# Performance work log

Measured on AMD Instinct MI355X. Metric: run time of the kernel, lower is better.

Reference implementation:

```python
import jax, jax.numpy as jnp
import numpy as np
from jax import lax

NB = 3          # num_fft_bins
BETA_SCALE = 0.1


def _conv(x, w, b):
    # x: [B,Ci,H,W], w: [Co,Ci,3,3] (torch OIHW), b: [Co]
    y = lax.conv_general_dilated(x, w, (1, 1), 'SAME',
                                 dimension_numbers=('NCHW', 'OIHW', 'NCHW'))
    return y + b[None, :, None, None]


def _global_mean_std(x):
    # x: [B,C,H,W] -> mean,std over C*H*W, unbiased std (torch default ddof=1)
    B = x.shape[0]
    xf = x.reshape(B, -1)
    return jnp.mean(xf, axis=1), jnp.std(xf, axis=1, ddof=1)


def _row_fft_features(x):
    # x: [B,C,H,W] -> [B,NB]
    B, C, H, W = x.shape
    spec = jnp.fft.rfft(x.reshape(B, C * H, W), axis=-1)
    power = spec.real ** 2 + spec.imag ** 2       # [B, C*H, F]
    pm = jnp.mean(power, axis=1)                  # [B, F]
    F = pm.shape[-1]
    bs = F // NB
    feats = []
    for k in range(NB):
        s = k * bs
        e = (k + 1) * bs if k < NB - 1 else F
        feats.append(jnp.mean(pm[:, s:e], axis=-1))
    feats = jnp.log1p(jnp.stack(feats, axis=1))   # [B, NB]
    return feats / (jnp.mean(feats, axis=1, keepdims=True) + 1e-6)


def reference(noisy, base_out, mem_clean, w1, b1, w2, b2, w3, b3, mw1, mb1, mw2, mb2):
    C = noisy.shape[1]
    # local residual CNN on [noisy, base_out]
    h = jax.nn.relu(_conv(jnp.concatenate([noisy, base_out], axis=1), w1, b1))
    h = jax.nn.relu(_conv(h, w2, b2))
    r = _conv(h, w3, b3)                          # [B,C,H,W]

    # hyper features: 6 global stats + 3*NB fft band features
    mn, sn = _global_mean_std(noisy)
    mb_, sb = _global_mean_std(base_out)
    mm, sm = _global_mean_std(mem_clean)
    feats = jnp.concatenate([
        jnp.stack([mn, sn, mb_, sb, mm, sm], axis=1),
        _row_fft_features(noisy),
        _row_fft_features(base_out),
        _row_fft_features(mem_clean),
    ], axis=1)                                    # [B, 6+3*NB]

    hid = jax.nn.relu(feats @ mw1.T + mb1)
    hyper = hid @ mw2.T + mb2                     # [B, 2C]
    gamma = jax.nn.sigmoid(hyper[:, :C])[:, :, None, None]
    beta = (BETA_SCALE * jnp.tanh(hyper[:, C:]))[:, :, None, None]

    out = base_out + gamma * r + beta
    return jnp.clip(out, 0.0, 1.0)


def setup_inputs() -> dict:
    key = jax.random.key(0)
    ks = jax.random.split(key, 16)
    B, C, H, W = 32, 1, 512, 512
    Hc = 16
    in_feat = 6 + 3 * NB
    s = 0.05
    return {
        'noisy': jax.random.uniform(ks[0], (B, C, H, W), jnp.float32),
        'base_out': jax.random.uniform(ks[1], (B, C, H, W), jnp.float32),
        'mem_clean': jax.random.uniform(ks[2], (B, C, H, W), jnp.float32),
        'w1': jax.random.normal(ks[3], (Hc, 2 * C, 3, 3), jnp.float32) * s,
        'b1': jax.random.normal(ks[4], (Hc,), jnp.float32) * s,
        'w2': jax.random.normal(ks[5], (Hc, Hc, 3, 3), jnp.float32) * s,
        'b2': jax.random.normal(ks[6], (Hc,), jnp.float32) * s,
        'w3': jax.random.normal(ks[7], (C, Hc, 3, 3), jnp.float32) * s,
        'b3': jax.random.normal(ks[8], (C,), jnp.float32) * s,
        'mw1': jax.random.normal(ks[9], (Hc, in_feat), jnp.float32) * s,
        'mb1': jax.random.normal(ks[10], (Hc,), jnp.float32) * s,
        'mw2': jax.random.normal(ks[11], (2 * C, Hc), jnp.float32) * s,
        'mb2': jax.random.normal(ks[12], (2 * C,), jnp.float32) * s,
    }
```

## Files before the change

kernel.cpp:

```cpp
#include <hip/hip_runtime.h>
#include <stdint.h>

typedef _Float16 h8_t __attribute__((ext_vector_type(8)));
typedef _Float16 h4_t __attribute__((ext_vector_type(4)));
typedef float f32x4 __attribute__((ext_vector_type(4)));

union H8 { h8_t v; uint32_t u[4]; _Float16 h[8]; };
union H4 { h4_t v; uint32_t u[2]; _Float16 h[4]; };

struct TrueT  { static constexpr bool value = true;  };
struct FalseT { static constexpr bool value = false; };

#define S1 584
#define S2 552


__global__ void zero_ws(double* wsd) {
    int i = threadIdx.x;
    if (i < 480)
        __hip_atomic_store(&wsd[i], 0.0, __ATOMIC_RELAXED, __HIP_MEMORY_SCOPE_AGENT);
}

__global__ __launch_bounds__(512) void fft_stats(const float* __restrict__ noisy,
                                                 const float* __restrict__ base,
                                                 const float* __restrict__ mem,
                                                 double* __restrict__ binacc,
                                                 double* __restrict__ stats) {
    int bid = blockIdx.x;
    int tid = threadIdx.x;
    int f   = tid >> 8;
    int t   = tid & 255;
    int rp  = ((bid & 127) << 1) | f;
    int b   = (bid >> 7) & 31;
    int iid = bid >> 12;
    const float* x = (iid == 0) ? noisy : (iid == 1) ? base : mem;
    const float* rowA = x + (((size_t)b << 9) + (rp << 1)) * 512;
    const float* rowB = rowA + 512;

    __shared__ float re[1024], im[1024];
    __shared__ float2 tw[256];
    __shared__ float sbins[3];
    __shared__ float swsum[8], swsq[8];
    const int fb = f << 9;

    if (tid < 256) {
        float ang = -6.2831853071795864769f * (float)tid * (1.f / 512.f);
        float sn, cs;
        __sincosf(ang, &sn, &cs);
        tw[tid] = make_float2(cs, sn);
    }

    float a0 = rowA[t], a1 = rowA[t + 256];
    float b0 = rowB[t], b1 = rowB[t + 256];

    int r0 = __brev((unsigned)t) >> 23;
    int r1 = __brev((unsigned)(t + 256)) >> 23;
    re[fb + r0] = a0; im[fb + r0] = b0;
    re[fb + r1] = a1; im[fb + r1] = b1;

    float ps = a0 + a1 + b0 + b1;
    float pq = a0 * a0 + a1 * a1 + b0 * b0 + b1 * b1;
    #pragma unroll
    for (int off = 32; off > 0; off >>= 1) {
        ps += __shfl_down(ps, off);
        pq += __shfl_down(pq, off);
    }
    if ((tid & 63) == 0) { swsum[tid >> 6] = ps; swsq[tid >> 6] = pq; }
    if (tid < 3) sbins[tid] = 0.f;
    __syncthreads();

    for (int s = 1; s <= 9; ++s) {
        int h = 1 << (s - 1);
        int pos = t & (h - 1);
        int grp = t >> (s - 1);
        int i0 = fb + (grp << s) + pos;
        int i1 = i0 + h;
        float2 w = tw[pos << (9 - s)];
        float cs = w.x, sn = w.y;
        float xr = re[i1], xi = im[i1];
        float tr = xr * cs - xi * sn;
        float ti = xr * sn + xi * cs;
        float ur = re[i0], ui = im[i0];
        re[i1] = ur - tr; im[i1] = ui - ti;
        re[i0] = ur + tr; im[i0] = ui + ti;
        __syncthreads();
    }

    for (int fq = t; fq <= 256; fq += 256) {
        int nf = (512 - fq) & 511;
        float zr = re[fb + fq], zi = im[fb + fq];
        float yr = re[fb + nf], yi = im[fb + nf];
        float ar = 0.5f * (zr + yr), ai = 0.5f * (zi - yi);
        float br = 0.5f * (zi + yi), bi = -0.5f * (zr - yr);
        float pw = ar * ar + ai * ai + br * br + bi * bi;
        int bin = (fq < 85) ? 0 : ((fq < 170) ? 1 : 2);
        atomicAdd(&sbins[bin], pw);
    }
    __syncthreads();
    if (tid < 3) atomicAdd(&binacc[(iid * 32 + b) * 3 + tid], (double)sbins[tid]);
    if (tid == 0) {
        float s8 = 0.f, q8 = 0.f;
        #pragma unroll
        for (int i = 0; i < 8; ++i) { s8 += swsum[i]; q8 += swsq[i]; }
        atomicAdd(&stats[(iid * 32 + b) * 2 + 0], (double)s8);
        atomicAdd(&stats[(iid * 32 + b) * 2 + 1], (double)q8);
    }
}

__global__ __launch_bounds__(256, 2) void conv_fused(
    const float* __restrict__ noisy, const float* __restrict__ base,
    const float* __restrict__ w1, const float* __restrict__ b1,
    const float* __restrict__ w2, const float* __restrict__ b2,
    const float* __restrict__ w3, const float* __restrict__ b3,
    const double* __restrict__ binacc, const double* __restrict__ stats,
    const float* __restrict__ mw1, const float* __restrict__ mb1,
    const float* __restrict__ mw2, const float* __restrict__ mb2,
    float* __restrict__ out) {

    __shared__ _Float16 sH1[36 * S1 + 32];
    __shared__ _Float16 sH2[34 * S2 + 32];
    __shared__ float sMLP[18];
    _Float16* sIn = sH2;

    const int tid = threadIdx.x;
    const int bid = blockIdx.x;
    const int bx = bid & 15, by = (bid >> 4) & 15, b = bid >> 8;
    const int oy0 = by * 32, ox0 = bx * 32;
    const int l = tid & 63, wave = tid >> 6;
    const int g = l >> 4, c15 = l & 15;
    const int t1 = g >> 1, e8 = (g & 1) << 3;
    const bool interior = ((unsigned)(bx - 1) < 14u) && ((unsigned)(by - 1) < 14u);

    if (tid < 16) {
        float feats[15];
        const double N = 262144.0;
        #pragma unroll
        for (int i = 0; i < 3; ++i) {
            const double* sp = &stats[(i * 32 + b) * 2];
            double s = __hip_atomic_load(&sp[0], __ATOMIC_RELAXED, __HIP_MEMORY_SCOPE_AGENT);
            double q = __hip_atomic_load(&sp[1], __ATOMIC_RELAXED, __HIP_MEMORY_SCOPE_AGENT);
            double mean = s / N;
            double var = (q - s * s / N) / (N - 1.0);
            feats[2 * i]     = (float)mean;
            feats[2 * i + 1] = sqrtf(fmaxf((float)var, 0.f));
        }
        const double cnt[3] = {85.0, 85.0, 87.0};
        #pragma unroll
        for (int i = 0; i < 3; ++i) {
            float fv[3]; float m = 0.f;
            #pragma unroll
            for (int k = 0; k < 3; ++k) {
                const double* bp = &binacc[(i * 32 + b) * 3 + k];
                double bv = __hip_atomic_load(bp, __ATOMIC_RELAXED, __HIP_MEMORY_SCOPE_AGENT);
                fv[k] = log1pf((float)(bv / (512.0 * cnt[k])));
                m += fv[k];
            }
            m = m * (1.f / 3.f);
            #pragma unroll
            for (int k = 0; k < 3; ++k) feats[6 + i * 3 + k] = fv[k] / (m + 1e-6f);
        }
        float a = mb1[tid];
        #pragma unroll
        for (int j = 0; j < 15; ++j) a += mw1[tid * 15 + j] * feats[j];
        sMLP[tid] = fmaxf(a, 0.f);
    }

    H8 wf1; H8 wf2[5]; H8 wf3[5];
    #pragma unroll
    for (int i = 0; i < 8; ++i) {
        int k = 8 * g + i;
        float wv = 0.f;
        if (k < 18) wv = w1[c15 * 18 + (k & 1) * 9 + (k >> 1)];
        wf1.h[i] = (_Float16)wv;
    }
    #pragma unroll
    for (int c = 0; c < 4; ++c) {
        int tap = 2 * c + t1;
        #pragma unroll
        for (int i = 0; i < 8; ++i) {
            int ci = e8 + i;
            wf2[c].h[i] = (_Float16)w2[c15 * 144 + ci * 9 + tap];
            float w3v = 0.f;
            if (c15 == 0) w3v = w3[ci * 9 + tap];
            wf3[c].h[i] = (_Float16)w3v;
        }
    }
    #pragma unroll
    for (int i = 0; i < 8; ++i) {
        float w2v = 0.f, w3v = 0.f;
        if (g < 2) {
            int ci = (g << 3) + i;
            w2v = w2[c15 * 144 + ci * 9 + 8];
            if (c15 == 0) w3v = w3[ci * 9 + 8];
        }
        wf2[4].h[i] = (_Float16)w2v;
        wf3[4].h[i] = (_Float16)w3v;
    }

    int offIn[4], off2[5], off3[5];
    #pragma unroll
    for (int j = 0; j < 4; ++j) {
        int tap = 4 * g + j;
        int dy = (tap * 171) >> 9;
        int dx = tap - 3 * dy;
        offIn[j] = (tap < 9) ? ((dy * 40 + dx) * 2) : 0;
    }
    #pragma unroll
    for (int c = 0; c < 5; ++c) {
        int tap = (c < 4) ? (2 * c + t1) : 8;
        int dy = (tap * 171) >> 9;
        int dx = tap - 3 * dy;
        int ci0 = (c < 4) ? e8 : (g << 3);
        off2[c] = dy * S1 + dx * 16 + ci0;
        off3[c] = dy * S2 + dx * 16 + ci0;
    }

    if (tid < 32) sH1[36 * S1 + tid] = (_Float16)0.f;
    else if (tid < 64) sH2[34 * S2 + (tid - 32)] = (_Float16)0.f;
    else if (tid < 100) {
        int r = tid - 64;
        #pragma unroll
        for (int i = 0; i < 8; ++i) sH1[r * S1 + 576 + i] = (_Float16)0.f;
    } else if (tid < 129) {
        int r = tid - 100 + 5;
        #pragma unroll
        for (int i = 0; i < 8; ++i) sH2[r * S2 + 544 + i] = (_Float16)0.f;
    }

    auto body = [&](auto tag) {
        constexpr bool INT = decltype(tag)::value;

        {
            const float* nB = noisy + ((size_t)b << 18);
            const float* bB = base + ((size_t)b << 18);
            for (int idx = tid; idx < 38 * 38; idx += 256) {
                unsigned iy = (unsigned)idx / 38u, ix = (unsigned)idx - iy * 38u;
                int gy = oy0 + (int)iy - 3, gx = ox0 + (int)ix - 3;
                float vn, vb;
                if constexpr (INT) {
                    int o = (gy << 9) + gx;
                    vn = nB[o]; vb = bB[o];
                } else {
                    vn = 0.f; vb = 0.f;
                    if ((unsigned)gy < 512u && (unsigned)gx < 512u) {
                        int o = (gy << 9) + gx;
                        vn = nB[o]; vb = bB[o];
                    }
                }
                union { uint32_t u; _Float16 h[2]; } pk;
                pk.h[0] = (_Float16)vn; pk.h[1] = (_Float16)vb;
                *(uint32_t*)&sIn[((int)iy * 40 + (int)ix) * 2] = pk.u;
            }
        }
        __syncthreads();

        {
            f32x4 binit;
            #pragma unroll
            for (int i = 0; i < 4; ++i) binit[i] = b1[4 * g + i];
            #pragma unroll
            for (int it = 0; it < 21; ++it) {
                int t = wave + 4 * it;
                unsigned p = (unsigned)(t * 16 + c15);
                bool valid = p < 1296u;
                if (p > 1295u) p = 1295u;
                unsigned y1 = p / 36u, x1 = p - y1 * 36u;
                int baseIn = (y1 * 40 + x1) * 2;
                H8 bf;
                #pragma unroll
                for (int j = 0; j < 4; ++j)
                    bf.u[j] = *(const uint32_t*)&sIn[baseIn + offIn[j]];
                f32x4 acc = __builtin_amdgcn_mfma_f32_16x16x32_f16(wf1.v, bf.v, binit, 0, 0, 0);
                H4 st;
                if constexpr (INT) {
                    #pragma unroll
                    for (int i = 0; i < 4; ++i) st.h[i] = (_Float16)fmaxf(acc[i], 0.f);
                } else {
                    int gy = oy0 + (int)y1 - 2, gx = ox0 + (int)x1 - 2;
                    bool inimg = ((unsigned)gy < 512u) && ((unsigned)gx < 512u);
                    #pragma unroll
                    for (int i = 0; i < 4; ++i)
                        st.h[i] = inimg ? (_Float16)fmaxf(acc[i], 0.f) : (_Float16)0.f;
                }
                if (valid)
                    *(h4_t*)&sH1[y1 * S1 + x1 * 16 + 4 * g] = st.v;
            }
        }
        __syncthreads();

        if (tid == 0) {
            float h0 = mb2[0], h1 = mb2[1];
            #pragma unroll
            for (int j = 0; j < 16; ++j) { h0 += mw2[j] * sMLP[j]; h1 += mw2[16 + j] * sMLP[j]; }
            sMLP[16] = 1.f / (1.f + expf(-h0));
            sMLP[17] = 0.1f * tanhf(h1);
        }

        {
            f32x4 binit;
            #pragma unroll
            for (int i = 0; i < 4; ++i) binit[i] = b2[4 * g + i];
            #pragma unroll
            for (int it = 0; it < 10; ++it) {
                int t = wave + 8 * it;
                int tB = t + 4;
                unsigned pA = (unsigned)(t * 16 + c15);  if (pA > 1155u) pA = 1155u;
                unsigned pB = (unsigned)(tB * 16 + c15); if (pB > 1155u) pB = 1155u;
                unsigned yA = pA / 34u, xA = pA - yA * 34u;
                unsigned yB = pB / 34u, xB = pB - yB * 34u;
                int baseA = (int)(yA * S1 + xA * 16);
                int baseB = (int)(yB * S1 + xB * 16);
                f32x4 accA = binit, accB = binit;
                #pragma unroll
                for (int c = 0; c < 5; ++c) {
                    H8 bfA, bfB;
                    bfA.v = *(const h8_t*)&sH1[baseA + off2[c]];
                    bfB.v = *(const h8_t*)&sH1[baseB + off2[c]];
                    accA = __builtin_amdgcn_mfma_f32_16x16x32_f16(wf2[c].v, bfA.v, accA, 0, 0, 0);
                    accB = __builtin_amdgcn_mfma_f32_16x16x32_f16(wf2[c].v, bfB.v, accB, 0, 0, 0);
                }
                if ((unsigned)(t * 16 + c15) < 1156u) {
                    H4 st;
                    if constexpr (INT) {
                        #pragma unroll
                        for (int i = 0; i < 4; ++i) st.h[i] = (_Float16)fmaxf(accA[i], 0.f);
                    } else {
                        int gy = oy0 + (int)yA - 1, gx = ox0 + (int)xA - 1;
                        bool inimg = ((unsigned)gy < 512u) && ((unsigned)gx < 512u);
                        #pragma unroll
                        for (int i = 0; i < 4; ++i)
                            st.h[i] = inimg ? (_Float16)fmaxf(accA[i], 0.f) : (_Float16)0.f;
                    }
                    *(h4_t*)&sH2[yA * S2 + xA * 16 + 4 * g] = st.v;
                }
                if ((unsigned)(tB * 16 + c15) < 1156u) {
                    H4 st;
                    if constexpr (INT) {
                        #pragma unroll
                        for (int i = 0; i < 4; ++i) st.h[i] = (_Float16)fmaxf(accB[i], 0.f);
                    } else {
                        int gy = oy0 + (int)yB - 1, gx = ox0 + (int)xB - 1;
                        bool inimg = ((unsigned)gy < 512u) && ((unsigned)gx < 512u);
                        #pragma unroll
                        for (int i = 0; i < 4; ++i)
                            st.h[i] = inimg ? (_Float16)fmaxf(accB[i], 0.f) : (_Float16)0.f;
                    }
                    *(h4_t*)&sH2[yB * S2 + xB * 16 + 4 * g] = st.v;
                }
            }
        }
        __syncthreads();

        {
            float b3v = b3[0];
            float gamma = sMLP[16], beta = sMLP[17];
            #pragma unroll
            for (int it = 0; it < 8; ++it) {
                int t = wave + 8 * it;
                int tB = t + 4;
                unsigned pA = (unsigned)(t * 16 + c15);
                unsigned pB = (unsigned)(tB * 16 + c15);
                unsigned yA = pA >> 5, xA = pA & 31u;
                unsigned yB = pB >> 5, xB = pB & 31u;
                int baseA = (int)(yA * S2 + xA * 16);
                int baseB = (int)(yB * S2 + xB * 16);
                f32x4 accA = {b3v, b3v, b3v, b3v};
                f32x4 accB = {b3v, b3v, b3v, b3v};
                #pragma unroll
                for (int c = 0; c < 5; ++c) {
                    H8 bfA, bfB;
                    bfA.v = *(const h8_t*)&sH2[baseA + off3[c]];
                    bfB.v = *(const h8_t*)&sH2[baseB + off3[c]];
                    accA = __builtin_amdgcn_mfma_f32_16x16x32_f16(wf3[c].v, bfA.v, accA, 0, 0, 0);
                    accB = __builtin_amdgcn_mfma_f32_16x16x32_f16(wf3[c].v, bfB.v, accB, 0, 0, 0);
                }
                if (l < 16) {
                    size_t oA = ((size_t)b << 18) + ((size_t)(oy0 + yA) << 9) + (ox0 + xA);
                    float o1 = fminf(fmaxf(base[oA] + gamma * accA[0] + beta, 0.f), 1.f);
                    out[oA] = o1;
                    size_t oB = ((size_t)b << 18) + ((size_t)(oy0 + yB) << 9) + (ox0 + xB);
                    float o2 = fminf(fmaxf(base[oB] + gamma * accB[0] + beta, 0.f), 1.f);
                    out[oB] = o2;
                }
            }
        }
    };

    if (interior) body(TrueT{});
    else          body(FalseT{});
}

extern "C" void kernel_launch(void* const* d_in, const int* in_sizes, int n_in,
                              void* d_out, int out_size, void* d_ws, size_t ws_size,
                              hipStream_t stream) {
    const float* noisy = (const float*)d_in[0];
    const float* base  = (const float*)d_in[1];
    const float* mem   = (const float*)d_in[2];
    const float* w1  = (const float*)d_in[3];
    const float* b1  = (const float*)d_in[4];
    const float* w2  = (const float*)d_in[5];
    const float* b2  = (const float*)d_in[6];
    const float* w3  = (const float*)d_in[7];
    const float* b3  = (const float*)d_in[8];
    const float* mw1 = (const float*)d_in[9];
    const float* mb1 = (const float*)d_in[10];
    const float* mw2 = (const float*)d_in[11];
    const float* mb2 = (const float*)d_in[12];

    double* wsd = (double*)d_ws;
    double* binacc = wsd;
    double* stats  = wsd + 288;
    float* out = (float*)d_out;

    hipLaunchKernelGGL(zero_ws, dim3(1), dim3(512), 0, stream, wsd);
    hipLaunchKernelGGL(fft_stats, dim3(3 * 32 * 128), dim3(512), 0, stream, noisy, base, mem, binacc, stats);
    hipLaunchKernelGGL(conv_fused, dim3(8192), dim3(256), 0, stream, noisy, base,
                       w1, b1, w2, b2, w3, b3, binacc, stats, mw1, mb1, mw2, mb2, out);
}
```

Measured before the change: 513.7 us.

## Replace radix-2 row FFT with radix-4 plus final radix-2 stage

The per-row FFT in the stats kernel changes from nine radix-2 stages to four radix-4 stages on two interleaved 256-point halves, followed by one radix-2 combine. This cuts the number of shared-memory passes and barriers. Each block now handles four row-pairs with float2 vector loads, which halves the grid size. The cost is more registers per thread, a larger shared-memory footprint, and more complex indexing.

```diff
diff --git a/kernel.cpp b/kernel.cpp
--- a/kernel.cpp
+++ b/kernel.cpp
@@ -28,38 +28,44 @@
                                                  double* __restrict__ stats) {
     int bid = blockIdx.x;
     int tid = threadIdx.x;
-    int f   = tid >> 8;
-    int t   = tid & 255;
-    int rp  = ((bid & 127) << 1) | f;
-    int b   = (bid >> 7) & 31;
-    int iid = bid >> 12;
+    int fi  = tid >> 7;
+    int w   = tid & 127;
+    int grp = bid & 63;
+    int b   = (bid >> 6) & 31;
+    int iid = bid >> 11;
+    int rp  = grp * 4 + fi;
     const float* x = (iid == 0) ? noisy : (iid == 1) ? base : mem;
-    const float* rowA = x + (((size_t)b << 9) + (rp << 1)) * 512;
-    const float* rowB = rowA + 512;
-
-    __shared__ float re[1024], im[1024];
-    __shared__ float2 tw[256];
+    const float2* rowA = (const float2*)(x + (((size_t)b << 9) + (rp << 1)) * 512);
+    const float2* rowB = rowA + 256;
+
+    __shared__ float re[2048], im[2048];
+    __shared__ float2 tw[512];
     __shared__ float sbins[3];
     __shared__ float swsum[8], swsq[8];
-    const int fb = f << 9;
-
-    if (tid < 256) {
+    const int fb = fi << 9;
+
+    {
         float ang = -6.2831853071795864769f * (float)tid * (1.f / 512.f);
         float sn, cs;
         __sincosf(ang, &sn, &cs);
         tw[tid] = make_float2(cs, sn);
     }
 
-    float a0 = rowA[t], a1 = rowA[t + 256];
-    float b0 = rowB[t], b1 = rowB[t + 256];
-
-    int r0 = __brev((unsigned)t) >> 23;
-    int r1 = __brev((unsigned)(t + 256)) >> 23;
-    re[fb + r0] = a0; im[fb + r0] = b0;
-    re[fb + r1] = a1; im[fb + r1] = b1;
-
-    float ps = a0 + a1 + b0 + b1;
-    float pq = a0 * a0 + a1 * a1 + b0 * b0 + b1 * b1;
+    float2 a01 = rowA[w], a23 = rowA[w + 128];
+    float2 b01 = rowB[w], b23 = rowB[w + 128];
+
+    auto rev4 = [](int n) {
+        return ((n & 3) << 6) | (((n >> 2) & 3) << 4) | (((n >> 4) & 3) << 2) | ((n >> 6) & 3);
+    };
+    int r0 = rev4(w), r1 = rev4(w + 128);
+    re[fb + r0]       = a01.x; im[fb + r0]       = b01.x;
+    re[fb + 256 + r0] = a01.y; im[fb + 256 + r0] = b01.y;
+    re[fb + r1]       = a23.x; im[fb + r1]       = b23.x;
+    re[fb + 256 + r1] = a23.y; im[fb + 256 + r1] = b23.y;
+
+    float ps = a01.x + a01.y + a23.x + a23.y + b01.x + b01.y + b23.x + b23.y;
+    float pq = a01.x*a01.x + a01.y*a01.y + a23.x*a23.x + a23.y*a23.y
+             + b01.x*b01.x + b01.y*b01.y + b23.x*b23.x + b23.y*b23.y;
     #pragma unroll
     for (int off = 32; off > 0; off >>= 1) {
         ps += __shfl_down(ps, off);
@@ -69,31 +75,57 @@
     if (tid < 3) sbins[tid] = 0.f;
     __syncthreads();
 
-    for (int s = 1; s <= 9; ++s) {
-        int h = 1 << (s - 1);
-        int pos = t & (h - 1);
-        int grp = t >> (s - 1);
-        int i0 = fb + (grp << s) + pos;
-        int i1 = i0 + h;
-        float2 w = tw[pos << (9 - s)];
-        float cs = w.x, sn = w.y;
-        float xr = re[i1], xi = im[i1];
-        float tr = xr * cs - xi * sn;
-        float ti = xr * sn + xi * cs;
-        float ur = re[i0], ui = im[i0];
-        re[i1] = ur - tr; im[i1] = ui - ti;
-        re[i0] = ur + tr; im[i0] = ui + ti;
+    const int sub = w >> 6, bi = w & 63;
+    const int sb = fb + sub * 256;
+    #pragma unroll
+    for (int s = 0; s < 4; ++s) {
+        int h = 1 << (2 * s);
+        int p = bi & (h - 1);
+        int g4 = bi >> (2 * s);
+        int i0 = sb + g4 * 4 * h + p;
+        int es = p * (128 >> (2 * s));
+        float2 w1 = tw[es], w2 = tw[2 * es], w3 = tw[3 * es];
+        float x0r = re[i0],         x0i = im[i0];
+        float a1r = re[i0 + h],     a1i = im[i0 + h];
+        float a2r = re[i0 + 2*h],   a2i = im[i0 + 2*h];
+        float a3r = re[i0 + 3*h],   a3i = im[i0 + 3*h];
+        float x1r = a1r * w1.x - a1i * w1.y, x1i = a1r * w1.y + a1i * w1.x;
+        float x2r = a2r * w2.x - a2i * w2.y, x2i = a2r * w2.y + a2i * w2.x;
+        float x3r = a3r * w3.x - a3i * w3.y, x3i = a3r * w3.y + a3i * w3.x;
+        float t0r = x0r + x2r, t0i = x0i + x2i;
+        float t1r = x0r - x2r, t1i = x0i - x2i;
+        float t2r = x1r + x3r, t2i = x1i + x3i;
+        float t3r = x1r - x3r, t3i = x1i - x3i;
+        re[i0]         = t0r + t2r; im[i0]         = t0i + t2i;
+        re[i0 + h]     = t1r + t3i; im[i0 + h]     = t1i - t3r;
+        re[i0 + 2*h]   = t0r - t2r; im[i0 + 2*h]   = t0i - t2i;
+        re[i0 + 3*h]   = t1r - t3i; im[i0 + 3*h]   = t1i + t3r;
         __syncthreads();
     }
 
-    for (int fq = t; fq <= 256; fq += 256) {
-        int nf = (512 - fq) & 511;
-        float zr = re[fb + fq], zi = im[fb + fq];
+    #pragma unroll
+    for (int kk = 0; kk < 2; ++kk) {
+        int k = w + kk * 128;
+        float er = re[fb + k],       ei = im[fb + k];
+        float orr = re[fb + 256 + k], oi = im[fb + 256 + k];
+        float2 wv = tw[k];
+        float tr = orr * wv.x - oi * wv.y, ti = orr * wv.y + oi * wv.x;
+        re[fb + k]       = er + tr; im[fb + k]       = ei + ti;
+        re[fb + 256 + k] = er - tr; im[fb + 256 + k] = ei - ti;
+    }
+    __syncthreads();
+
+    #pragma unroll
+    for (int ii = 0; ii < 3; ++ii) {
+        if (ii == 2 && w != 0) break;
+        int f = (ii == 0) ? w : ((ii == 1) ? w + 128 : 256);
+        int nf = (512 - f) & 511;
+        float zr = re[fb + f], zi = im[fb + f];
         float yr = re[fb + nf], yi = im[fb + nf];
         float ar = 0.5f * (zr + yr), ai = 0.5f * (zi - yi);
-        float br = 0.5f * (zi + yi), bi = -0.5f * (zr - yr);
-        float pw = ar * ar + ai * ai + br * br + bi * bi;
-        int bin = (fq < 85) ? 0 : ((fq < 170) ? 1 : 2);
+        float br = 0.5f * (zi + yi), bi2 = -0.5f * (zr - yr);
+        float pw = ar * ar + ai * ai + br * br + bi2 * bi2;
+        int bin = (f < 85) ? 0 : ((f < 170) ? 1 : 2);
         atomicAdd(&sbins[bin], pw);
     }
     __syncthreads();
@@ -413,7 +445,7 @@
     float* out = (float*)d_out;
 
     hipLaunchKernelGGL(zero_ws, dim3(1), dim3(512), 0, stream, wsd);
-    hipLaunchKernelGGL(fft_stats, dim3(3 * 32 * 128), dim3(512), 0, stream, noisy, base, mem, binacc, stats);
+    hipLaunchKernelGGL(fft_stats, dim3(3 * 32 * 64), dim3(512), 0, stream, noisy, base, mem, binacc, stats);
     hipLaunchKernelGGL(conv_fused, dim3(8192), dim3(256), 0, stream, noisy, base,
                        w1, b1, w2, b2, w3, b3, binacc, stats, mw1, mb1, mw2, mb2, out);
 }
```

Result: faster. 472.4 us (-8.1%).
